# Optimization experiments

Measured on AMD Instinct MI355X. Metric: run time of the kernel, lower is better.

## Reference

```python
import jax, jax.numpy as jnp
import numpy as np

B, S, D, H, F, E, TOPK, W = 1, 4096, 768, 12, 3072, 7, 2, 256  # W = one-sided window


def _layer_norm(x, g, b, eps=1e-5):
    m = jnp.mean(x, -1, keepdims=True)
    v = jnp.var(x, -1, keepdims=True)
    return (x - m) * jax.lax.rsqrt(v + eps) * g + b


def _sliding_attn(x, Wq, bq, Wk, bk, Wv, bv):
    # Longformer sliding-window attention, chunked (no dense SxS matrix).
    Bx, Sx, Dx = x.shape
    Dh = Dx // H
    def proj(Wm, bm):
        return (x @ Wm + bm).reshape(Bx, Sx, H, Dh).transpose(0, 2, 1, 3)  # [B,H,S,Dh]
    q = proj(Wq, bq) * (1.0 / np.sqrt(Dh))
    k = proj(Wk, bk)
    v = proj(Wv, bv)
    nc = Sx // W
    kp = jnp.pad(k, ((0, 0), (0, 0), (W, W), (0, 0)))
    vp = jnp.pad(v, ((0, 0), (0, 0), (W, W), (0, 0)))
    # each query chunk of W tokens sees a 3W key window
    idx = (jnp.arange(nc) * W)[:, None] + jnp.arange(3 * W)[None, :]  # [nc,3W]
    kc = kp[:, :, idx]  # [B,H,nc,3W,Dh]
    vc = vp[:, :, idx]
    qc = q.reshape(Bx, H, nc, W, Dh)
    scores = jnp.einsum('bhcqd,bhckd->bhcqk', qc, kc)  # [B,H,nc,W,3W]
    qi = jnp.arange(W)[:, None]
    ki = jnp.arange(3 * W)[None, :]
    band = (ki >= qi) & (ki <= qi + 2 * W)  # |key_pos - query_pos| <= W
    pos = (jnp.arange(nc) * W)[:, None, None] + ki[None] - W  # global key pos
    valid = band[None] & (pos >= 0) & (pos < Sx)  # [nc,W,3W]
    scores = jnp.where(valid[None, None], scores, -1e9)
    probs = jax.nn.softmax(scores, axis=-1)
    out = jnp.einsum('bhcqk,bhckd->bhcqd', probs, vc)
    return out.reshape(Bx, H, Sx, Dh).transpose(0, 2, 1, 3).reshape(Bx, Sx, Dx)


def setup_inputs() -> dict:
    key = jax.random.key(0)
    ks = jax.random.split(key, 16)
    sc = 0.02
    rn = lambda k, shp: jax.random.normal(k, shp, jnp.float32) * sc
    return {
        'hidden_states': jax.random.normal(ks[0], (B, S, D), jnp.float32),
        'Wq': rn(ks[1], (D, D)), 'bq': jnp.zeros((D,), jnp.float32),
        'Wk': rn(ks[2], (D, D)), 'bk': jnp.zeros((D,), jnp.float32),
        'Wv': rn(ks[3], (D, D)), 'bv': jnp.zeros((D,), jnp.float32),
        'Wo': rn(ks[4], (D, D)), 'bo': jnp.zeros((D,), jnp.float32),
        'ln1_g': jnp.ones((D,), jnp.float32), 'ln1_b': jnp.zeros((D,), jnp.float32),
        'gate_W': rn(ks[5], (D, E)), 'gate_b': jnp.zeros((E,), jnp.float32),
        'W1e': rn(ks[6], (E, D, F)), 'b1e': jnp.zeros((E, F), jnp.float32),
        'W2e': rn(ks[7], (E, F, D)), 'b2e': jnp.zeros((E, D), jnp.float32),
        'Wd': rn(ks[8], (D, D)), 'bd': jnp.zeros((D,), jnp.float32),
        'ln2_g': jnp.ones((D,), jnp.float32), 'ln2_b': jnp.zeros((D,), jnp.float32),
    }


def reference(hidden_states, Wq, bq, Wk, bk, Wv, bv, Wo, bo, ln1_g, ln1_b,
              gate_W, gate_b, W1e, b1e, W2e, b2e, Wd, bd, ln2_g, ln2_b):
    # attention + SelfOutput (dense + residual + LN); dropout = identity (eval)
    attn = _sliding_attn(hidden_states, Wq, bq, Wk, bk, Wv, bv)
    attention_output = _layer_norm(attn @ Wo + bo + hidden_states, ln1_g, ln1_b)
    # MoE feed-forward: dense all-experts compute, top-k masked softmax gate
    gate_logits = attention_output @ gate_W + gate_b  # [B,S,E]
    topv, topi = jax.lax.top_k(gate_logits, TOPK)
    # softmax over (-inf scatter of topk) == softmax over topk values scattered back
    sw = jax.nn.softmax(topv, axis=-1)  # [B,S,k]
    gate_weights = jnp.einsum('bske,bsk->bse',
                              jax.nn.one_hot(topi, E, dtype=attention_output.dtype), sw)
    h = jax.nn.gelu(jnp.einsum('bsd,edf->bsef', attention_output, W1e) + b1e,
                    approximate=False)  # [B,S,E,F]
    eo = jnp.einsum('bsef,efd->bsed', h, W2e) + b2e  # [B,S,E,D]
    moe = jnp.einsum('bsed,bse->bsd', eo, gate_weights)
    ffn = moe @ Wd + bd
    layer_output = _layer_norm(ffn + attention_output, ln2_g, ln2_b)
    return layer_output, gate_weights
```

## Files before the change

### kernel.cpp

```cpp
#include <hip/hip_runtime.h>
#include <math.h>

#define S_LEN 4096
#define DMODEL 768
#define NHEADS 12
#define DH 64
#define FDIM 3072
#define NEXP 7
#define NPAIR (2*S_LEN)
#define MAXTILES 40

typedef _Float16 f16x8 __attribute__((ext_vector_type(8)));
typedef float f32x4 __attribute__((ext_vector_type(4)));

__device__ __forceinline__ unsigned short f2h(float f){
  union { _Float16 h; unsigned short u; } v; v.h = (_Float16)f; return v.u;
}
__device__ __forceinline__ float gelu_f(float x){
  return 0.5f * x * (1.0f + erff(x * 0.7071067811865475f));
}
__device__ __forceinline__ f32x4 mfma16(f16x8 a, f16x8 b, f32x4 c){
  return __builtin_amdgcn_mfma_f32_16x16x32_f16(a, b, c, 0, 0, 0);
}
__device__ __forceinline__ void glds16(const void* g, void* l){
  __builtin_amdgcn_global_load_lds((const __attribute__((address_space(1))) unsigned*)g,
                                   (__attribute__((address_space(3))) unsigned*)l, 16, 0, 0);
}

__global__ __launch_bounds__(256) void split_kernel(const float* __restrict__ in,
    unsigned short* __restrict__ out, int n){
  int i = blockIdx.x*256 + threadIdx.x;
  if (i >= n) return;
  out[i] = f2h(in[i]);
}

__global__ __launch_bounds__(256) void transp_kernel(const float* __restrict__ in,
    unsigned short* __restrict__ out,
    int R, int C, long inStride, long outStride){
  const float* ip = in + (long)blockIdx.z * inStride;
  long ob = (long)blockIdx.z * outStride;
  __shared__ float tile[32][33];
  int c0 = blockIdx.x*32, r0 = blockIdx.y*32;
  int tx = threadIdx.x, ty = threadIdx.y;
  for (int i = ty; i < 32; i += 8)
    tile[i][tx] = ip[(long)(r0+i)*C + c0 + tx];
  __syncthreads();
  int t  = tx + ty*32;
  int sx = t & 15;
  int sc = t >> 4;
  #pragma unroll
  for (int j = 0; j < 2; j++){
    int cc = sc + j*16;
    float v0 = tile[sx*2][cc], v1 = tile[sx*2+1][cc];
    long oidx = ob + (long)(c0+cc)*R + r0 + sx*2;
    unsigned uh = (unsigned)f2h(v0) | ((unsigned)f2h(v1) << 16);
    *(unsigned*)(out + oidx) = uh;
  }
}

struct GemmP {
  const unsigned short* A;
  const unsigned short* B;
  int M, N, K;
  const float* bias;  const float* bias2; const float* bias3;
  const float* resid;
  float* outF;
  unsigned short* outBF;
  unsigned short *qh,*kh,*vth;
  const int* pair_token;
  const float* pair_w;
  const int* cnt;
  const int* offs;
  const int* tile_e;
  const int* tile_m;
  const int* ntiles;
};

template<int MODE>
__global__ __launch_bounds__(256, 2) void gemm_bt(GemmP p){
  const int tid  = threadIdx.x;
  const int lane = tid & 63;
  const int wave = tid >> 6;
  const int quad = lane >> 4;
  const int ln   = lane & 15;
  const int wr = wave >> 1, wc = wave & 1;
  const int bn0 = blockIdx.x * 128;
  const int bm0 = blockIdx.y * 128;
  const int K = p.K;

  long aoff[2]; long boff[2]; int koff[2];
  #pragma unroll
  for (int j = 0; j < 2; j++){
    int c = tid + j*256;
    int row = c >> 2;
    koff[j] = (c & 3) * 8;
    aoff[j] = (long)(bm0 + row) * K;
    boff[j] = (long)(bn0 + row) * K;
  }

  __shared__ __align__(16) unsigned short As[2][128*32];
  __shared__ __align__(16) unsigned short Bs[2][128*32];

  auto stage = [&](int k0, int buf){
    #pragma unroll
    for (int j = 0; j < 2; j++){
      int c = tid + j*256;
      glds16(p.A + aoff[j] + k0 + koff[j], &As[buf][c*8]);
      glds16(p.B + boff[j] + k0 + koff[j], &Bs[buf][c*8]);
    }
  };

  f32x4 zero4 = {0.f, 0.f, 0.f, 0.f};
  f32x4 acc[4][4];
  #pragma unroll
  for (int i = 0; i < 4; i++)
    #pragma unroll
    for (int j = 0; j < 4; j++) acc[i][j] = zero4;

  stage(0, 0);
  __syncthreads();
  int cur = 0;

  for (int k0 = 0; k0 < K; k0 += 32){
    if (k0 + 32 < K) stage(k0 + 32, cur ^ 1);
    f16x8 af[4], bfr[4];
    #pragma unroll
    for (int mt = 0; mt < 4; mt++)
      af[mt] = *(const f16x8*)&As[cur][(wr*64 + mt*16 + ln)*32 + quad*8];
    #pragma unroll
    for (int nt = 0; nt < 4; nt++)
      bfr[nt] = *(const f16x8*)&Bs[cur][(wc*64 + nt*16 + ln)*32 + quad*8];
    #pragma unroll
    for (int mt = 0; mt < 4; mt++)
      #pragma unroll
      for (int nt = 0; nt < 4; nt++)
        acc[mt][nt] = mfma16(af[mt], bfr[nt], acc[mt][nt]);
    __syncthreads();
    cur ^= 1;
  }

  #pragma unroll
  for (int mt = 0; mt < 4; mt++){
    #pragma unroll
    for (int nt = 0; nt < 4; nt++){
      #pragma unroll
      for (int r = 0; r < 4; r++){
        int gm = bm0 + wr*64 + mt*16 + quad*4 + r;
        int gn = bn0 + wc*64 + nt*16 + ln;
        float v = acc[mt][nt][r];
        if (MODE == 0){
          int which = gn >= 1536 ? 2 : (gn >= 768 ? 1 : 0);
          int nn = gn - which*768;
          int hh = nn >> 6, dh = nn & 63;
          if (which == 0){
            float q = (v + p.bias[nn]) * 0.125f;
            long o = ((long)hh*S_LEN + gm)*64 + dh;
            p.qh[o] = f2h(q);
          } else if (which == 1){
            float kv = v + p.bias2[nn];
            long o = ((long)hh*S_LEN + gm)*64 + dh;
            p.kh[o] = f2h(kv);
          } else {
            float vv = v + p.bias3[nn];
            long o = ((long)hh*64 + dh)*S_LEN + gm;
            p.vth[o] = f2h(vv);
          }
        } else if (MODE == 1 || MODE == 4){
          long i = (long)gm*DMODEL + gn;
          p.outF[i] = v + p.bias[gn] + p.resid[i];
        }
      }
    }
  }
}

template<int MODE>
__global__ __launch_bounds__(512, 4) void gemm_big(GemmP p){
  const int ty = blockIdx.y;
  if (ty >= *p.ntiles) return;
  const int e   = p.tile_e[ty];
  const int bm0 = p.tile_m[ty];

  const int tid  = threadIdx.x;
  const int lane = tid & 63;
  const int wave = tid >> 6;
  const int quad = lane >> 4;
  const int ln   = lane & 15;
  const int wr = wave >> 1, wc = wave & 1;
  const int bn0 = blockIdx.x * 128;
  const int K = p.K;

  const int eoff = p.offs[e];
  const int Mloc = p.cnt[e];
  const unsigned short* Bp = p.B + (long)e * FDIM * DMODEL;

  long aoff[2]; int koffA[2];
  #pragma unroll
  for (int j = 0; j < 2; j++){
    int c = tid + j*512;
    int row = c >> 2;
    koffA[j] = (c & 3) * 8;
    int r = bm0 + row; if (r >= Mloc) r = Mloc - 1;
    aoff[j] = (MODE == 2) ? (long)p.pair_token[eoff + r] * K : (long)(eoff + r) * K;
  }
  long boff; int koffB;
  {
    int row = tid >> 2;
    koffB = (tid & 3) * 8;
    boff = (long)(bn0 + row) * K;
  }

  __shared__ __align__(16) unsigned short As[2][256*32];
  __shared__ __align__(16) unsigned short Bs[2][128*32];

  auto stage = [&](int k0, int buf){
    #pragma unroll
    for (int j = 0; j < 2; j++){
      int c = tid + j*512;
      glds16(p.A + aoff[j] + k0 + koffA[j], &As[buf][c*8]);
    }
    glds16(Bp + boff + k0 + koffB, &Bs[buf][tid*8]);
  };

  f32x4 zero4 = {0.f, 0.f, 0.f, 0.f};
  f32x4 acc[4][4];
  #pragma unroll
  for (int i = 0; i < 4; i++)
    #pragma unroll
    for (int j = 0; j < 4; j++) acc[i][j] = zero4;

  stage(0, 0);
  __syncthreads();
  int cur = 0;

  for (int k0 = 0; k0 < K; k0 += 32){
    if (k0 + 32 < K) stage(k0 + 32, cur ^ 1);
    f16x8 af[4], bfr[4];
    #pragma unroll
    for (int mt = 0; mt < 4; mt++)
      af[mt] = *(const f16x8*)&As[cur][(wr*64 + mt*16 + ln)*32 + quad*8];
    #pragma unroll
    for (int nt = 0; nt < 4; nt++)
      bfr[nt] = *(const f16x8*)&Bs[cur][(wc*64 + nt*16 + ln)*32 + quad*8];
    #pragma unroll
    for (int mt = 0; mt < 4; mt++)
      #pragma unroll
      for (int nt = 0; nt < 4; nt++)
        acc[mt][nt] = mfma16(af[mt], bfr[nt], acc[mt][nt]);
    __syncthreads();
    cur ^= 1;
  }

  #pragma unroll
  for (int mt = 0; mt < 4; mt++){
    #pragma unroll
    for (int nt = 0; nt < 4; nt++){
      #pragma unroll
      for (int r = 0; r < 4; r++){
        int gm = bm0 + wr*64 + mt*16 + quad*4 + r;
        int gn = bn0 + wc*64 + nt*16 + ln;
        if (gm < Mloc){
          float v = acc[mt][nt][r];
          if (MODE == 2){
            v = gelu_f(v + p.bias[(long)e*FDIM + gn]);
            p.outBF[(long)(eoff + gm)*FDIM + gn] = f2h(v);
          } else {
            int pi = eoff + gm;
            p.outF[(long)pi*DMODEL + gn] = v + p.bias[(long)e*DMODEL + gn];
          }
        }
      }
    }
  }
}

__global__ __launch_bounds__(256) void attn_mfma(
    const unsigned short* __restrict__ Qh,
    const unsigned short* __restrict__ Kh,
    const unsigned short* __restrict__ Vth,
    unsigned short* __restrict__ attn_h){
  const int c = blockIdx.x, h = blockIdx.y, qb = blockIdx.z;
  const int tid = threadIdx.x;
  const int lane = tid & 63, w = tid >> 6;
  const int quad = lane >> 4, ln = lane & 15;
  const int q0 = c*256 + qb*64;
  const int qw = q0 + w*16;

  __shared__ __align__(16) unsigned short Ks[64*64];
  __shared__ __align__(16) unsigned short Vs[64*64];
  __shared__ __align__(16) unsigned short Ps[4][16*72];

  f16x8 qf[2];
  {
    long qrow = ((long)h*S_LEN + qw + ln)*64 + quad*8;
    qf[0] = *(const f16x8*)(Qh + qrow);
    qf[1] = *(const f16x8*)(Qh + qrow + 32);
  }

  float m_s[4], l_s[4];
  f32x4 Oc[4];
  f32x4 z4 = {0.f,0.f,0.f,0.f};
  #pragma unroll
  for (int r = 0; r < 4; r++){ m_s[r] = -1e30f; l_s[r] = 0.f; }
  #pragma unroll
  for (int nt = 0; nt < 4; nt++) Oc[nt] = z4;

  const unsigned short* KB = Kh + (long)h*S_LEN*64;
  const unsigned short* VB = Vth + (long)h*64*S_LEN;

  for (int kb = 0; kb < 12; kb++){
    const int kstart = c*256 - 256 + kb*64;
    if (kstart + 63 < 0 || kstart >= S_LEN) continue;
    if (kstart + 63 < q0 - 256 || kstart > q0 + 63 + 256) continue;
    __syncthreads();
    #pragma unroll
    for (int p2 = 0; p2 < 2; p2++){
      int idx = p2*256 + tid;
      int row = idx >> 3;
      int pc  = idx & 7;
      int lc  = pc ^ (row & 7);
      int ka = kstart + row;
      int kac = ka < 0 ? 0 : (ka > S_LEN-1 ? S_LEN-1 : ka);
      long gK = (long)kac*64 + lc*8;
      glds16(KB + gK, &Ks[idx*8]);
      int ks0 = kstart + lc*8;
      ks0 = ks0 < 0 ? 0 : (ks0 > S_LEN-8 ? S_LEN-8 : ks0);
      long gV = (long)row*S_LEN + ks0;
      glds16(VB + gV, &Vs[idx*8]);
    }
    __syncthreads();
    if (kstart + 63 < qw - 256 || kstart > qw + 15 + 256) continue;

    f32x4 Sc[4];
    #pragma unroll
    for (int nt = 0; nt < 4; nt++) Sc[nt] = z4;
    #pragma unroll
    for (int kc = 0; kc < 2; kc++){
      f16x8 bh[4];
      #pragma unroll
      for (int nt = 0; nt < 4; nt++){
        int row = nt*16 + ln;
        int o = row*64 + (((kc*4 + quad) ^ (row & 7))*8);
        bh[nt] = *(const f16x8*)&Ks[o];
      }
      #pragma unroll
      for (int nt = 0; nt < 4; nt++)
        Sc[nt] = mfma16(qf[kc], bh[nt], Sc[nt]);
    }
    bool interior = (kstart >= qw - 241) && (kstart <= qw + 193) &&
                    (kstart >= 0) && (kstart + 63 <= S_LEN - 1);
    if (!interior){
      #pragma unroll
      for (int nt = 0; nt < 4; nt++){
        int ka = kstart + nt*16 + ln;
        #pragma unroll
        for (int r = 0; r < 4; r++){
          int qa = qw + quad*4 + r;
          bool v = (ka >= 0) && (ka < S_LEN) && (ka >= qa - 256) && (ka <= qa + 256);
          if (!v) Sc[nt][r] = -3.0e38f;
        }
      }
    }
    float bm[4];
    #pragma unroll
    for (int r = 0; r < 4; r++)
      bm[r] = fmaxf(fmaxf(Sc[0][r], Sc[1][r]), fmaxf(Sc[2][r], Sc[3][r]));
    #pragma unroll
    for (int off = 1; off < 16; off <<= 1)
      #pragma unroll
      for (int r = 0; r < 4; r++) bm[r] = fmaxf(bm[r], __shfl_xor(bm[r], off));
    float al[4];
    #pragma unroll
    for (int r = 0; r < 4; r++){
      float mnew = fmaxf(m_s[r], bm[r]);
      al[r] = __expf(m_s[r] - mnew);
      m_s[r] = mnew;
    }
    float psum[4] = {0.f,0.f,0.f,0.f};
    #pragma unroll
    for (int nt = 0; nt < 4; nt++){
      #pragma unroll
      for (int r = 0; r < 4; r++){
        float pv = __expf(Sc[nt][r] - m_s[r]);
        psum[r] += pv;
        int o = (quad*4 + r)*72 + nt*16 + ln;
        Ps[w][o] = f2h(pv);
      }
    }
    #pragma unroll
    for (int off = 1; off < 16; off <<= 1)
      #pragma unroll
      for (int r = 0; r < 4; r++) psum[r] += __shfl_xor(psum[r], off);
    #pragma unroll
    for (int r = 0; r < 4; r++) l_s[r] = l_s[r]*al[r] + psum[r];
    #pragma unroll
    for (int nt = 0; nt < 4; nt++)
      #pragma unroll
      for (int r = 0; r < 4; r++) Oc[nt][r] *= al[r];
    asm volatile("s_waitcnt lgkmcnt(0)" ::: "memory");
    #pragma unroll
    for (int kc = 0; kc < 2; kc++){
      f16x8 ph = *(const f16x8*)&Ps[w][ln*72 + kc*32 + quad*8];
      #pragma unroll
      for (int nt = 0; nt < 4; nt++){
        int row = nt*16 + ln;
        int o = row*64 + (((kc*4 + quad) ^ (row & 7))*8);
        f16x8 vh = *(const f16x8*)&Vs[o];
        Oc[nt] = mfma16(ph, vh, Oc[nt]);
      }
    }
  }
  float inv[4];
  #pragma unroll
  for (int r = 0; r < 4; r++) inv[r] = 1.f / l_s[r];
  #pragma unroll
  for (int nt = 0; nt < 4; nt++){
    #pragma unroll
    for (int r = 0; r < 4; r++){
      int qa = qw + quad*4 + r;
      long o = (long)qa*DMODEL + h*64 + nt*16 + ln;
      attn_h[o] = f2h(Oc[nt][r] * inv[r]);
    }
  }
}

__global__ __launch_bounds__(256) void ln_kernel(const float* __restrict__ x,
    const float* __restrict__ g, const float* __restrict__ b,
    float* __restrict__ outF, unsigned short* __restrict__ outH){
  int s = blockIdx.x;
  const float* row = x + (long)s*DMODEL;
  int t = threadIdx.x;
  float v0 = row[t], v1 = row[t+256], v2 = row[t+512];
  float sum = v0+v1+v2;
  float sq  = v0*v0 + v1*v1 + v2*v2;
  for (int o = 32; o > 0; o >>= 1){ sum += __shfl_xor(sum, o); sq += __shfl_xor(sq, o); }
  __shared__ float s1[4], s2[4];
  int wv = t >> 6;
  if ((t & 63) == 0){ s1[wv] = sum; s2[wv] = sq; }
  __syncthreads();
  sum = s1[0]+s1[1]+s1[2]+s1[3];
  sq  = s2[0]+s2[1]+s2[2]+s2[3];
  float mean = sum * (1.0f/DMODEL);
  float var  = sq  * (1.0f/DMODEL) - mean*mean;
  float inv = rsqrtf(var + 1e-5f);
  float* orow = outF + (long)s*DMODEL;
  unsigned short* hrow = outH ? outH + (long)s*DMODEL : (unsigned short*)0;
  #pragma unroll
  for (int j = 0; j < 3; j++){
    int d = t + j*256;
    float y = (row[d] - mean) * inv * g[d] + b[d];
    orow[d] = y;
    if (hrow) hrow[d] = f2h(y);
  }
}

__global__ __launch_bounds__(256) void gate_kernel(const float* __restrict__ x,
    const float* __restrict__ gw, const float* __restrict__ gb,
    float* __restrict__ gate_out, int* __restrict__ tok_e,
    float* __restrict__ tok_w){
  int w = threadIdx.x >> 6;
  int lane = threadIdx.x & 63;
  int s = blockIdx.x*4 + w;
  float acc[NEXP];
  #pragma unroll
  for (int e = 0; e < NEXP; e++) acc[e] = 0.f;
  const float* xr = x + (long)s*DMODEL;
  #pragma unroll
  for (int j = 0; j < DMODEL/64; j++){
    int d = lane + j*64;
    float xv = xr[d];
    const float* wr = gw + (long)d*NEXP;
    #pragma unroll
    for (int e = 0; e < NEXP; e++) acc[e] += xv * wr[e];
  }
  #pragma unroll
  for (int e = 0; e < NEXP; e++){
    float v = acc[e];
    for (int o = 32; o > 0; o >>= 1) v += __shfl_xor(v, o);
    acc[e] = v;
  }
  if (lane == 0){
    #pragma unroll
    for (int e = 0; e < NEXP; e++) acc[e] += gb[e];
    int i0 = 0;
    for (int e = 1; e < NEXP; e++) if (acc[e] > acc[i0]) i0 = e;
    int i1 = -1;
    for (int e = 0; e < NEXP; e++) if (e != i0 && (i1 < 0 || acc[e] > acc[i1])) i1 = e;
    float e1 = expf(acc[i1] - acc[i0]);
    float inv = 1.f / (1.f + e1);
    float w0 = inv, w1 = e1 * inv;
    float* go = gate_out + (long)s*NEXP;
    #pragma unroll
    for (int e = 0; e < NEXP; e++) go[e] = 0.f;
    go[i0] = w0; go[i1] = w1;
    tok_e[s*2] = i0; tok_e[s*2+1] = i1;
    tok_w[s*2] = w0; tok_w[s*2+1] = w1;
  }
}

__global__ __launch_bounds__(256) void route_kernel(const int* __restrict__ tok_e,
    const float* __restrict__ tok_w,
    int* __restrict__ cnt, int* __restrict__ offs,
    int* __restrict__ pair_token, float* __restrict__ pair_w, int* __restrict__ tok_pi,
    int* __restrict__ tile_e, int* __restrict__ tile_m, int* __restrict__ ntiles){
  __shared__ int hist[256][NEXP];
  __shared__ int cntS[NEXP], offsS[NEXP];
  const int t = threadIdx.x;
  const int CH = NPAIR/256;
  const int base = t*CH;
  #pragma unroll
  for (int e = 0; e < NEXP; e++) hist[t][e] = 0;
  for (int i = 0; i < CH; i++)
    hist[t][tok_e[base+i]]++;
  __syncthreads();
  if (t < NEXP){
    int s = 0;
    for (int i = 0; i < 256; i++){ int v = hist[i][t]; hist[i][t] = s; s += v; }
    cntS[t] = s;
  }
  __syncthreads();
  if (t == 0){
    int s = 0, tt = 0;
    for (int e = 0; e < NEXP; e++){ offsS[e] = s; s += cntS[e]; }
    for (int e = 0; e < NEXP; e++)
      for (int m0 = 0; m0 < cntS[e]; m0 += 256){ tile_e[tt] = e; tile_m[tt] = m0; tt++; }
    *ntiles = tt;
    for (int e = 0; e < NEXP; e++){ cnt[e] = cntS[e]; offs[e] = offsS[e]; }
  }
  __syncthreads();
  for (int i = 0; i < CH; i++){
    int idx = base + i;
    int e = tok_e[idx];
    int pi = offsS[e] + hist[t][e]++;
    pair_token[pi] = idx >> 1;
    pair_w[pi] = tok_w[idx];
    tok_pi[idx] = pi;
  }
}

__global__ __launch_bounds__(256) void combine_kernel(const float* __restrict__ Pbuf,
    const int* __restrict__ tok_pi, const float* __restrict__ tok_w,
    unsigned short* __restrict__ moe_h){
  int t = blockIdx.x;
  int d = threadIdx.x;
  float w0 = tok_w[t*2], w1 = tok_w[t*2+1];
  long p0 = (long)tok_pi[t*2]   * DMODEL;
  long p1 = (long)tok_pi[t*2+1] * DMODEL;
  unsigned short* orow = moe_h + (long)t*DMODEL;
  #pragma unroll
  for (int j = 0; j < 3; j++){
    int dd = d + j*256;
    orow[dd] = f2h(w0*Pbuf[p0+dd] + w1*Pbuf[p1+dd]);
  }
}

extern "C" void kernel_launch(void* const* d_in, const int* in_sizes, int n_in,
                              void* d_out, int out_size, void* d_ws, size_t ws_size,
                              hipStream_t stream){
  (void)in_sizes; (void)n_in; (void)out_size; (void)ws_size;
  const float* hidden = (const float*)d_in[0];
  const float* Wq  = (const float*)d_in[1];
  const float* bq  = (const float*)d_in[2];
  const float* Wk  = (const float*)d_in[3];
  const float* bk  = (const float*)d_in[4];
  const float* Wv  = (const float*)d_in[5];
  const float* bv  = (const float*)d_in[6];
  const float* Wo  = (const float*)d_in[7];
  const float* bo  = (const float*)d_in[8];
  const float* ln1g = (const float*)d_in[9];
  const float* ln1b = (const float*)d_in[10];
  const float* gateW = (const float*)d_in[11];
  const float* gateB = (const float*)d_in[12];
  const float* W1e = (const float*)d_in[13];
  const float* b1e = (const float*)d_in[14];
  const float* W2e = (const float*)d_in[15];
  const float* b2e = (const float*)d_in[16];
  const float* Wd  = (const float*)d_in[17];
  const float* bd  = (const float*)d_in[18];
  const float* ln2g = (const float*)d_in[19];
  const float* ln2b = (const float*)d_in[20];

  float* outL = (float*)d_out;
  float* outG = outL + (size_t)S_LEN*DMODEL;

  const size_t SD = (size_t)S_LEN*DMODEL;
  char* base = (char*)d_ws;
  size_t off = 0;
  auto alloc = [&](size_t bytes)->void*{
    void* r = base + off;
    off = (off + bytes + 255) & ~(size_t)255;
    return r;
  };
  unsigned short* x_h     = (unsigned short*)alloc(SD*2);
  unsigned short* wqkv_h  = (unsigned short*)alloc((size_t)2304*768*2);
  unsigned short* wo_h    = (unsigned short*)alloc((size_t)768*768*2);
  unsigned short* wd_h    = (unsigned short*)alloc((size_t)768*768*2);
  unsigned short* w1_h    = (unsigned short*)alloc((size_t)NEXP*FDIM*DMODEL*2);
  unsigned short* w2_h    = (unsigned short*)alloc((size_t)NEXP*FDIM*DMODEL*2);
  unsigned short* q_h   = (unsigned short*)alloc(SD*2);
  unsigned short* k_h   = (unsigned short*)alloc(SD*2);
  unsigned short* vt_h  = (unsigned short*)alloc(SD*2);
  unsigned short* attn_h = (unsigned short*)alloc(SD*2);
  float* preLN1    = (float*)alloc(SD*4);
  float* attnout_f = (float*)alloc(SD*4);
  unsigned short* attnout_h = (unsigned short*)alloc(SD*2);
  int*   tok_e = (int*)alloc(2*S_LEN*4);
  float* tok_w = (float*)alloc(2*S_LEN*4);
  int*   tok_pi = (int*)alloc(2*S_LEN*4);
  int*   cnt   = (int*)alloc(32*4);
  int*   offs  = (int*)alloc(32*4);
  int*   tile_e = (int*)alloc(MAXTILES*4);
  int*   tile_m = (int*)alloc(MAXTILES*4);
  int*   ntiles = (int*)alloc(4);
  int*   pair_token = (int*)alloc(NPAIR*4);
  float* pair_w     = (float*)alloc(NPAIR*4);
  unsigned short* Hbuf = (unsigned short*)alloc((size_t)NPAIR*FDIM*2);
  float* Pbuf = (float*)alloc((size_t)NPAIR*DMODEL*4);
  unsigned short* moe_h = (unsigned short*)alloc(SD*2);
  float* preLN2 = preLN1;

  split_kernel<<<dim3((unsigned)(SD/256)), dim3(256), 0, stream>>>(hidden, x_h, (int)SD);
  transp_kernel<<<dim3(24,24,1), dim3(32,8), 0, stream>>>(Wq, wqkv_h,           DMODEL, DMODEL, 0, 0);
  transp_kernel<<<dim3(24,24,1), dim3(32,8), 0, stream>>>(Wk, wqkv_h+768*768,   DMODEL, DMODEL, 0, 0);
  transp_kernel<<<dim3(24,24,1), dim3(32,8), 0, stream>>>(Wv, wqkv_h+2*768*768, DMODEL, DMODEL, 0, 0);
  transp_kernel<<<dim3(24,24,1), dim3(32,8), 0, stream>>>(Wo, wo_h, DMODEL, DMODEL, 0, 0);
  transp_kernel<<<dim3(24,24,1), dim3(32,8), 0, stream>>>(Wd, wd_h, DMODEL, DMODEL, 0, 0);
  transp_kernel<<<dim3(96,24,NEXP), dim3(32,8), 0, stream>>>(W1e, w1_h, DMODEL, FDIM, (long)DMODEL*FDIM, (long)DMODEL*FDIM);
  transp_kernel<<<dim3(24,96,NEXP), dim3(32,8), 0, stream>>>(W2e, w2_h, FDIM, DMODEL, (long)DMODEL*FDIM, (long)DMODEL*FDIM);

  GemmP pq = {};
  pq.A = x_h; pq.B = wqkv_h;
  pq.M = S_LEN; pq.N = 2304; pq.K = DMODEL;
  pq.bias = bq; pq.bias2 = bk; pq.bias3 = bv;
  pq.qh = q_h; pq.kh = k_h; pq.vth = vt_h;
  gemm_bt<0><<<dim3(18,32,1), dim3(256), 0, stream>>>(pq);

  attn_mfma<<<dim3(16,NHEADS,4), dim3(256), 0, stream>>>(q_h, k_h, vt_h, attn_h);

  GemmP pw = {};
  pw.A = attn_h; pw.B = wo_h;
  pw.M = S_LEN; pw.N = DMODEL; pw.K = DMODEL;
  pw.bias = bo; pw.resid = hidden; pw.outF = preLN1;
  gemm_bt<1><<<dim3(6,32,1), dim3(256), 0, stream>>>(pw);

  ln_kernel<<<dim3(S_LEN), dim3(256), 0, stream>>>(preLN1, ln1g, ln1b, attnout_f, attnout_h);

  gate_kernel<<<dim3(S_LEN/4), dim3(256), 0, stream>>>(attnout_f, gateW, gateB, outG, tok_e, tok_w);
  route_kernel<<<dim3(1), dim3(256), 0, stream>>>(tok_e, tok_w, cnt, offs,
      pair_token, pair_w, tok_pi, tile_e, tile_m, ntiles);

  GemmP p1 = {};
  p1.A = attnout_h; p1.B = w1_h; p1.M = S_LEN; p1.N = FDIM; p1.K = DMODEL;
  p1.bias = b1e; p1.outBF = Hbuf;
  p1.pair_token = pair_token; p1.cnt = cnt; p1.offs = offs;
  p1.tile_e = tile_e; p1.tile_m = tile_m; p1.ntiles = ntiles;
  gemm_big<2><<<dim3(24,MAXTILES), dim3(512), 0, stream>>>(p1);

  GemmP p2 = {};
  p2.A = Hbuf; p2.B = w2_h; p2.M = S_LEN; p2.N = DMODEL; p2.K = FDIM;
  p2.bias = b2e; p2.outF = Pbuf;
  p2.pair_token = pair_token; p2.pair_w = pair_w; p2.cnt = cnt; p2.offs = offs;
  p2.tile_e = tile_e; p2.tile_m = tile_m; p2.ntiles = ntiles;
  gemm_big<3><<<dim3(6,MAXTILES), dim3(512), 0, stream>>>(p2);

  combine_kernel<<<dim3(S_LEN), dim3(256), 0, stream>>>(Pbuf, tok_pi, tok_w, moe_h);
  GemmP pd = {};
  pd.A = moe_h; pd.B = wd_h; pd.M = S_LEN; pd.N = DMODEL; pd.K = DMODEL;
  pd.bias = bd; pd.resid = attnout_f; pd.outF = preLN2;
  gemm_bt<4><<<dim3(6,32,1), dim3(256), 0, stream>>>(pd);

  ln_kernel<<<dim3(S_LEN), dim3(256), 0, stream>>>(preLN2, ln2g, ln2b, outL, nullptr);
}
```

Before: 609.5 us.

## Deepen GEMM prefetch pipeline, swizzle LDS layout, and remap blocks across XCDs

Both GEMM kernels now prefetch two K-steps ahead, using explicit vmcnt waits and split barriers in place of a single __syncthreads. That lets global-to-LDS loads overlap MFMA work instead of draining every iteration. The K-chunk offset within each LDS row is XOR-swizzled by row to reduce bank conflicts on the fragment reads. Block indices are also remapped so neighbouring tiles land on the same XCD for better L2 reuse. The hand-written waitcnt counts are fragile and assume the grid size divides by 8.

```diff
diff --git a/kernel.cpp b/kernel.cpp
--- a/kernel.cpp
+++ b/kernel.cpp
@@ -25,6 +25,10 @@
 __device__ __forceinline__ void glds16(const void* g, void* l){
   __builtin_amdgcn_global_load_lds((const __attribute__((address_space(1))) unsigned*)g,
                                    (__attribute__((address_space(3))) unsigned*)l, 16, 0, 0);
+}
+__device__ __forceinline__ int xcd_logical(int lin, int total){
+  int q = total >> 3;
+  return (lin & 7)*q + (lin >> 3);
 }
 
 __global__ __launch_bounds__(256) void split_kernel(const float* __restrict__ in,
@@ -84,8 +88,10 @@
   const int quad = lane >> 4;
   const int ln   = lane & 15;
   const int wr = wave >> 1, wc = wave & 1;
-  const int bn0 = blockIdx.x * 128;
-  const int bm0 = blockIdx.y * 128;
+  const int lin = blockIdx.y * gridDim.x + blockIdx.x;
+  const int logical = xcd_logical(lin, gridDim.x*gridDim.y);
+  const int bn0 = (logical % gridDim.x) * 128;
+  const int bm0 = (logical / gridDim.x) * 128;
   const int K = p.K;
 
   long aoff[2]; long boff[2]; int koff[2];
@@ -93,7 +99,8 @@
   for (int j = 0; j < 2; j++){
     int c = tid + j*256;
     int row = c >> 2;
-    koff[j] = (c & 3) * 8;
+    int pc  = c & 3;
+    koff[j] = ((pc ^ (row & 3)) * 8);
     aoff[j] = (long)(bm0 + row) * K;
     boff[j] = (long)(bn0 + row) * K;
   }
@@ -118,24 +125,33 @@
     for (int j = 0; j < 4; j++) acc[i][j] = zero4;
 
   stage(0, 0);
-  __syncthreads();
+  stage(32, 1);
   int cur = 0;
 
   for (int k0 = 0; k0 < K; k0 += 32){
-    if (k0 + 32 < K) stage(k0 + 32, cur ^ 1);
+    if (k0 + 32 < K) { asm volatile("s_waitcnt vmcnt(4)" ::: "memory"); }
+    else             { asm volatile("s_waitcnt vmcnt(0)" ::: "memory"); }
+    __builtin_amdgcn_sched_barrier(0);
+    __builtin_amdgcn_s_barrier();
+
     f16x8 af[4], bfr[4];
     #pragma unroll
     for (int mt = 0; mt < 4; mt++)
-      af[mt] = *(const f16x8*)&As[cur][(wr*64 + mt*16 + ln)*32 + quad*8];
+      af[mt] = *(const f16x8*)&As[cur][(wr*64 + mt*16 + ln)*32 + ((quad ^ (ln & 3))*8)];
     #pragma unroll
     for (int nt = 0; nt < 4; nt++)
-      bfr[nt] = *(const f16x8*)&Bs[cur][(wc*64 + nt*16 + ln)*32 + quad*8];
+      bfr[nt] = *(const f16x8*)&Bs[cur][(wc*64 + nt*16 + ln)*32 + ((quad ^ (ln & 3))*8)];
+    asm volatile("s_waitcnt lgkmcnt(0)" ::: "memory");
+    __builtin_amdgcn_sched_barrier(0);
+    __builtin_amdgcn_s_barrier();
+
+    if (k0 + 64 < K) stage(k0 + 64, cur);
+
     #pragma unroll
     for (int mt = 0; mt < 4; mt++)
       #pragma unroll
       for (int nt = 0; nt < 4; nt++)
         acc[mt][nt] = mfma16(af[mt], bfr[nt], acc[mt][nt]);
-    __syncthreads();
     cur ^= 1;
   }
 
@@ -176,7 +192,10 @@
 
 template<int MODE>
 __global__ __launch_bounds__(512, 4) void gemm_big(GemmP p){
-  const int ty = blockIdx.y;
+  const int lin = blockIdx.y * gridDim.x + blockIdx.x;
+  const int logical = xcd_logical(lin, gridDim.x*gridDim.y);
+  const int bx = logical % gridDim.x;
+  const int ty = logical / gridDim.x;
   if (ty >= *p.ntiles) return;
   const int e   = p.tile_e[ty];
   const int bm0 = p.tile_m[ty];
@@ -187,7 +206,7 @@
   const int quad = lane >> 4;
   const int ln   = lane & 15;
   const int wr = wave >> 1, wc = wave & 1;
-  const int bn0 = blockIdx.x * 128;
+  const int bn0 = bx * 128;
   const int K = p.K;
 
   const int eoff = p.offs[e];
@@ -199,14 +218,16 @@
   for (int j = 0; j < 2; j++){
     int c = tid + j*512;
     int row = c >> 2;
-    koffA[j] = (c & 3) * 8;
+    int pc  = c & 3;
+    koffA[j] = ((pc ^ (row & 3)) * 8);
     int r = bm0 + row; if (r >= Mloc) r = Mloc - 1;
     aoff[j] = (MODE == 2) ? (long)p.pair_token[eoff + r] * K : (long)(eoff + r) * K;
   }
   long boff; int koffB;
   {
     int row = tid >> 2;
-    koffB = (tid & 3) * 8;
+    int pc  = tid & 3;
+    koffB = ((pc ^ (row & 3)) * 8);
     boff = (long)(bn0 + row) * K;
   }
 
@@ -230,24 +251,33 @@
     for (int j = 0; j < 4; j++) acc[i][j] = zero4;
 
   stage(0, 0);
-  __syncthreads();
+  stage(32, 1);
   int cur = 0;
 
   for (int k0 = 0; k0 < K; k0 += 32){
-    if (k0 + 32 < K) stage(k0 + 32, cur ^ 1);
+    if (k0 + 32 < K) { asm volatile("s_waitcnt vmcnt(3)" ::: "memory"); }
+    else             { asm volatile("s_waitcnt vmcnt(0)" ::: "memory"); }
+    __builtin_amdgcn_sched_barrier(0);
+    __builtin_amdgcn_s_barrier();
+
     f16x8 af[4], bfr[4];
     #pragma unroll
     for (int mt = 0; mt < 4; mt++)
-      af[mt] = *(const f16x8*)&As[cur][(wr*64 + mt*16 + ln)*32 + quad*8];
+      af[mt] = *(const f16x8*)&As[cur][(wr*64 + mt*16 + ln)*32 + ((quad ^ (ln & 3))*8)];
     #pragma unroll
     for (int nt = 0; nt < 4; nt++)
-      bfr[nt] = *(const f16x8*)&Bs[cur][(wc*64 + nt*16 + ln)*32 + quad*8];
+      bfr[nt] = *(const f16x8*)&Bs[cur][(wc*64 + nt*16 + ln)*32 + ((quad ^ (ln & 3))*8)];
+    asm volatile("s_waitcnt lgkmcnt(0)" ::: "memory");
+    __builtin_amdgcn_sched_barrier(0);
+    __builtin_amdgcn_s_barrier();
+
+    if (k0 + 64 < K) stage(k0 + 64, cur);
+
     #pragma unroll
     for (int mt = 0; mt < 4; mt++)
       #pragma unroll
       for (int nt = 0; nt < 4; nt++)
         acc[mt][nt] = mfma16(af[mt], bfr[nt], acc[mt][nt]);
-    __syncthreads();
     cur ^= 1;
   }
 
```

New measurement: 589.2 us. 1.03x faster.

## Unify GEMMs into one triple-buffered 256x128 kernel with XCD-aware block remap

Applied to the files above, without the earlier changes.

Replaces the separate dense and grouped-expert GEMM kernels with one templated kernel. It uses 256x128 output tiles computed by 4 waves, each covering 128x64. LDS gets three stages with explicit vmcnt waits and raw barriers, and register fragments are double-buffered so LDS reads for the next k-step overlap the current MFMAs. Block indices are remapped so neighbouring tiles land on the same XCD for L2 reuse, and s_setprio raises priority around the MFMA bursts. The costs are much higher register pressure, more LDS per block, and fewer blocks for the small 768-wide GEMMs.

```diff
diff --git a/kernel.cpp b/kernel.cpp
--- a/kernel.cpp
+++ b/kernel.cpp
@@ -25,6 +25,10 @@
 __device__ __forceinline__ void glds16(const void* g, void* l){
   __builtin_amdgcn_global_load_lds((const __attribute__((address_space(1))) unsigned*)g,
                                    (__attribute__((address_space(3))) unsigned*)l, 16, 0, 0);
+}
+__device__ __forceinline__ int xcd_logical(int lin, int total){
+  int q = total >> 3;
+  return (lin & 7)*q + (lin >> 3);
 }
 
 __global__ __launch_bounds__(256) void split_kernel(const float* __restrict__ in,
@@ -77,75 +81,135 @@
 };
 
 template<int MODE>
-__global__ __launch_bounds__(256, 2) void gemm_bt(GemmP p){
+__global__ __launch_bounds__(256, 2) void gemm_new(GemmP p){
   const int tid  = threadIdx.x;
   const int lane = tid & 63;
   const int wave = tid >> 6;
   const int quad = lane >> 4;
   const int ln   = lane & 15;
   const int wr = wave >> 1, wc = wave & 1;
-  const int bn0 = blockIdx.x * 128;
-  const int bm0 = blockIdx.y * 128;
-  const int K = p.K;
-
-  long aoff[2]; long boff[2]; int koff[2];
+
+  int bx, byy;
+  {
+    const int lin = blockIdx.y * gridDim.x + blockIdx.x;
+    const int logical = xcd_logical(lin, gridDim.x*gridDim.y);
+    bx  = logical % gridDim.x;
+    byy = logical / gridDim.x;
+  }
+  int e = 0, bm0, Mloc = 1<<30, eoff = 0;
+  const unsigned short* Bbase = p.B;
+  if (MODE == 2 || MODE == 3){
+    if (byy >= *p.ntiles) return;
+    e    = p.tile_e[byy];
+    bm0  = p.tile_m[byy];
+    eoff = p.offs[e];
+    Mloc = p.cnt[e];
+    Bbase = p.B + (long)e * FDIM * DMODEL;
+  } else {
+    bm0 = byy * 256;
+  }
+  const int bn0 = bx * 128;
+  const int K  = p.K;
+  const int nk = K >> 5;
+
+  long aoff[4]; int kca[4];
+  #pragma unroll
+  for (int j = 0; j < 4; j++){
+    int c = tid + j*256;
+    int row = c >> 2;
+    kca[j] = (c & 3) * 8;
+    int r = bm0 + row;
+    if (MODE == 2){ if (r >= Mloc) r = Mloc - 1; aoff[j] = (long)p.pair_token[eoff + r] * K; }
+    else if (MODE == 3){ if (r >= Mloc) r = Mloc - 1; aoff[j] = (long)(eoff + r) * K; }
+    else aoff[j] = (long)r * K;
+  }
+  long boff[2]; int kcb[2];
   #pragma unroll
   for (int j = 0; j < 2; j++){
     int c = tid + j*256;
     int row = c >> 2;
-    koff[j] = (c & 3) * 8;
-    aoff[j] = (long)(bm0 + row) * K;
+    kcb[j] = (c & 3) * 8;
     boff[j] = (long)(bn0 + row) * K;
   }
 
-  __shared__ __align__(16) unsigned short As[2][128*32];
-  __shared__ __align__(16) unsigned short Bs[2][128*32];
+  __shared__ __align__(16) unsigned short As[3][256*32];
+  __shared__ __align__(16) unsigned short Bs[3][128*32];
 
   auto stage = [&](int k0, int buf){
     #pragma unroll
-    for (int j = 0; j < 2; j++){
-      int c = tid + j*256;
-      glds16(p.A + aoff[j] + k0 + koff[j], &As[buf][c*8]);
-      glds16(p.B + boff[j] + k0 + koff[j], &Bs[buf][c*8]);
-    }
+    for (int j = 0; j < 4; j++)
+      glds16(p.A + aoff[j] + k0 + kca[j], &As[buf][(tid + j*256)*8]);
+    #pragma unroll
+    for (int j = 0; j < 2; j++)
+      glds16(Bbase + boff[j] + k0 + kcb[j], &Bs[buf][(tid + j*256)*8]);
   };
 
   f32x4 zero4 = {0.f, 0.f, 0.f, 0.f};
-  f32x4 acc[4][4];
-  #pragma unroll
-  for (int i = 0; i < 4; i++)
+  f32x4 acc[8][4];
+  #pragma unroll
+  for (int i = 0; i < 8; i++)
     #pragma unroll
     for (int j = 0; j < 4; j++) acc[i][j] = zero4;
 
   stage(0, 0);
-  __syncthreads();
-  int cur = 0;
-
-  for (int k0 = 0; k0 < K; k0 += 32){
-    if (k0 + 32 < K) stage(k0 + 32, cur ^ 1);
-    f16x8 af[4], bfr[4];
-    #pragma unroll
-    for (int mt = 0; mt < 4; mt++)
-      af[mt] = *(const f16x8*)&As[cur][(wr*64 + mt*16 + ln)*32 + quad*8];
-    #pragma unroll
-    for (int nt = 0; nt < 4; nt++)
-      bfr[nt] = *(const f16x8*)&Bs[cur][(wc*64 + nt*16 + ln)*32 + quad*8];
-    #pragma unroll
-    for (int mt = 0; mt < 4; mt++)
-      #pragma unroll
-      for (int nt = 0; nt < 4; nt++)
-        acc[mt][nt] = mfma16(af[mt], bfr[nt], acc[mt][nt]);
-    __syncthreads();
-    cur ^= 1;
-  }
-
-  #pragma unroll
-  for (int mt = 0; mt < 4; mt++){
+  stage(32, 1);
+  stage(64, 2);
+  asm volatile("s_waitcnt vmcnt(12)" ::: "memory");
+  __builtin_amdgcn_sched_barrier(0);
+  __builtin_amdgcn_s_barrier();
+  __builtin_amdgcn_sched_barrier(0);
+
+  f16x8 aC[8], bC[4], aN[8], bN[4];
+  #pragma unroll
+  for (int mt = 0; mt < 8; mt++)
+    aC[mt] = *(const f16x8*)&As[0][(wr*128 + mt*16 + ln)*32 + quad*8];
+  #pragma unroll
+  for (int nt = 0; nt < 4; nt++)
+    bC[nt] = *(const f16x8*)&Bs[0][(wc*64 + nt*16 + ln)*32 + quad*8];
+
+#define SUBITER(i, FCA, FCB, FNA, FNB) do { \
+    int s_ = t + (i); \
+    if (s_ + 1 < nk){ \
+      if (s_ + 2 < nk) { asm volatile("s_waitcnt vmcnt(6)" ::: "memory"); } \
+      else             { asm volatile("s_waitcnt vmcnt(0)" ::: "memory"); } \
+      asm volatile("s_waitcnt lgkmcnt(0)" ::: "memory"); \
+      __builtin_amdgcn_sched_barrier(0); \
+      __builtin_amdgcn_s_barrier(); \
+      __builtin_amdgcn_sched_barrier(0); \
+      if (s_ + 3 < nk) stage((s_+3)*32, (i)%3); \
+      _Pragma("unroll") \
+      for (int mt = 0; mt < 8; mt++) \
+        FNA[mt] = *(const f16x8*)&As[((i)+1)%3][(wr*128 + mt*16 + ln)*32 + quad*8]; \
+      _Pragma("unroll") \
+      for (int nt = 0; nt < 4; nt++) \
+        FNB[nt] = *(const f16x8*)&Bs[((i)+1)%3][(wc*64 + nt*16 + ln)*32 + quad*8]; \
+    } \
+    __builtin_amdgcn_s_setprio(1); \
+    _Pragma("unroll") \
+    for (int mt = 0; mt < 8; mt++) \
+      _Pragma("unroll") \
+      for (int nt = 0; nt < 4; nt++) \
+        acc[mt][nt] = mfma16(FCA[mt], FCB[nt], acc[mt][nt]); \
+    __builtin_amdgcn_s_setprio(0); \
+  } while(0)
+
+  for (int t = 0; t < nk; t += 6){
+    SUBITER(0, aC, bC, aN, bN);
+    SUBITER(1, aN, bN, aC, bC);
+    SUBITER(2, aC, bC, aN, bN);
+    SUBITER(3, aN, bN, aC, bC);
+    SUBITER(4, aC, bC, aN, bN);
+    SUBITER(5, aN, bN, aC, bC);
+  }
+#undef SUBITER
+
+  #pragma unroll
+  for (int mt = 0; mt < 8; mt++){
     #pragma unroll
     for (int nt = 0; nt < 4; nt++){
       #pragma unroll
       for (int r = 0; r < 4; r++){
-        int gm = bm0 + wr*64 + mt*16 + quad*4 + r;
+        int gm = bm0 + wr*128 + mt*16 + quad*4 + r;
         int gn = bn0 + wc*64 + nt*16 + ln;
         float v = acc[mt][nt][r];
         if (MODE == 0){
@@ -168,103 +232,13 @@
         } else if (MODE == 1 || MODE == 4){
           long i = (long)gm*DMODEL + gn;
           p.outF[i] = v + p.bias[gn] + p.resid[i];
-        }
-      }
-    }
-  }
-}
-
-template<int MODE>
-__global__ __launch_bounds__(512, 4) void gemm_big(GemmP p){
-  const int ty = blockIdx.y;
-  if (ty >= *p.ntiles) return;
-  const int e   = p.tile_e[ty];
-  const int bm0 = p.tile_m[ty];
-
-  const int tid  = threadIdx.x;
-  const int lane = tid & 63;
-  const int wave = tid >> 6;
-  const int quad = lane >> 4;
-  const int ln   = lane & 15;
-  const int wr = wave >> 1, wc = wave & 1;
-  const int bn0 = blockIdx.x * 128;
-  const int K = p.K;
-
-  const int eoff = p.offs[e];
-  const int Mloc = p.cnt[e];
-  const unsigned short* Bp = p.B + (long)e * FDIM * DMODEL;
-
-  long aoff[2]; int koffA[2];
-  #pragma unroll
-  for (int j = 0; j < 2; j++){
-    int c = tid + j*512;
-    int row = c >> 2;
-    koffA[j] = (c & 3) * 8;
-    int r = bm0 + row; if (r >= Mloc) r = Mloc - 1;
-    aoff[j] = (MODE == 2) ? (long)p.pair_token[eoff + r] * K : (long)(eoff + r) * K;
-  }
-  long boff; int koffB;
-  {
-    int row = tid >> 2;
-    koffB = (tid & 3) * 8;
-    boff = (long)(bn0 + row) * K;
-  }
-
-  __shared__ __align__(16) unsigned short As[2][256*32];
-  __shared__ __align__(16) unsigned short Bs[2][128*32];
-
-  auto stage = [&](int k0, int buf){
-    #pragma unroll
-    for (int j = 0; j < 2; j++){
-      int c = tid + j*512;
-      glds16(p.A + aoff[j] + k0 + koffA[j], &As[buf][c*8]);
-    }
-    glds16(Bp + boff + k0 + koffB, &Bs[buf][tid*8]);
-  };
-
-  f32x4 zero4 = {0.f, 0.f, 0.f, 0.f};
-  f32x4 acc[4][4];
-  #pragma unroll
-  for (int i = 0; i < 4; i++)
-    #pragma unroll
-    for (int j = 0; j < 4; j++) acc[i][j] = zero4;
-
-  stage(0, 0);
-  __syncthreads();
-  int cur = 0;
-
-  for (int k0 = 0; k0 < K; k0 += 32){
-    if (k0 + 32 < K) stage(k0 + 32, cur ^ 1);
-    f16x8 af[4], bfr[4];
-    #pragma unroll
-    for (int mt = 0; mt < 4; mt++)
-      af[mt] = *(const f16x8*)&As[cur][(wr*64 + mt*16 + ln)*32 + quad*8];
-    #pragma unroll
-    for (int nt = 0; nt < 4; nt++)
-      bfr[nt] = *(const f16x8*)&Bs[cur][(wc*64 + nt*16 + ln)*32 + quad*8];
-    #pragma unroll
-    for (int mt = 0; mt < 4; mt++)
-      #pragma unroll
-      for (int nt = 0; nt < 4; nt++)
-        acc[mt][nt] = mfma16(af[mt], bfr[nt], acc[mt][nt]);
-    __syncthreads();
-    cur ^= 1;
-  }
-
-  #pragma unroll
-  for (int mt = 0; mt < 4; mt++){
-    #pragma unroll
-    for (int nt = 0; nt < 4; nt++){
-      #pragma unroll
-      for (int r = 0; r < 4; r++){
-        int gm = bm0 + wr*64 + mt*16 + quad*4 + r;
-        int gn = bn0 + wc*64 + nt*16 + ln;
-        if (gm < Mloc){
-          float v = acc[mt][nt][r];
-          if (MODE == 2){
-            v = gelu_f(v + p.bias[(long)e*FDIM + gn]);
-            p.outBF[(long)(eoff + gm)*FDIM + gn] = f2h(v);
-          } else {
+        } else if (MODE == 2){
+          if (gm < Mloc){
+            float g = gelu_f(v + p.bias[(long)e*FDIM + gn]);
+            p.outBF[(long)(eoff + gm)*FDIM + gn] = f2h(g);
+          }
+        } else {
+          if (gm < Mloc){
             int pi = eoff + gm;
             p.outF[(long)pi*DMODEL + gn] = v + p.bias[(long)e*DMODEL + gn];
           }
@@ -633,7 +607,7 @@
   pq.M = S_LEN; pq.N = 2304; pq.K = DMODEL;
   pq.bias = bq; pq.bias2 = bk; pq.bias3 = bv;
   pq.qh = q_h; pq.kh = k_h; pq.vth = vt_h;
-  gemm_bt<0><<<dim3(18,32,1), dim3(256), 0, stream>>>(pq);
+  gemm_new<0><<<dim3(18,16,1), dim3(256), 0, stream>>>(pq);
 
   attn_mfma<<<dim3(16,NHEADS,4), dim3(256), 0, stream>>>(q_h, k_h, vt_h, attn_h);
 
@@ -641,7 +615,7 @@
   pw.A = attn_h; pw.B = wo_h;
   pw.M = S_LEN; pw.N = DMODEL; pw.K = DMODEL;
   pw.bias = bo; pw.resid = hidden; pw.outF = preLN1;
-  gemm_bt<1><<<dim3(6,32,1), dim3(256), 0, stream>>>(pw);
+  gemm_new<1><<<dim3(6,16,1), dim3(256), 0, stream>>>(pw);
 
   ln_kernel<<<dim3(S_LEN), dim3(256), 0, stream>>>(preLN1, ln1g, ln1b, attnout_f, attnout_h);
 
@@ -654,20 +628,20 @@
   p1.bias = b1e; p1.outBF = Hbuf;
   p1.pair_token = pair_token; p1.cnt = cnt; p1.offs = offs;
   p1.tile_e = tile_e; p1.tile_m = tile_m; p1.ntiles = ntiles;
-  gemm_big<2><<<dim3(24,MAXTILES), dim3(512), 0, stream>>>(p1);
+  gemm_new<2><<<dim3(24,MAXTILES), dim3(256), 0, stream>>>(p1);
 
   GemmP p2 = {};
   p2.A = Hbuf; p2.B = w2_h; p2.M = S_LEN; p2.N = DMODEL; p2.K = FDIM;
   p2.bias = b2e; p2.outF = Pbuf;
   p2.pair_token = pair_token; p2.pair_w = pair_w; p2.cnt = cnt; p2.offs = offs;
   p2.tile_e = tile_e; p2.tile_m = tile_m; p2.ntiles = ntiles;
-  gemm_big<3><<<dim3(6,MAXTILES), dim3(512), 0, stream>>>(p2);
+  gemm_new<3><<<dim3(6,MAXTILES), dim3(256), 0, stream>>>(p2);
 
   combine_kernel<<<dim3(S_LEN), dim3(256), 0, stream>>>(Pbuf, tok_pi, tok_w, moe_h);
   GemmP pd = {};
   pd.A = moe_h; pd.B = wd_h; pd.M = S_LEN; pd.N = DMODEL; pd.K = DMODEL;
   pd.bias = bd; pd.resid = attnout_f; pd.outF = preLN2;
-  gemm_bt<4><<<dim3(6,32,1), dim3(256), 0, stream>>>(pd);
+  gemm_new<4><<<dim3(6,16,1), dim3(256), 0, stream>>>(pd);
 
   ln_kernel<<<dim3(S_LEN), dim3(256), 0, stream>>>(preLN2, ln2g, ln2b, outL, nullptr);
 }
```

Measured after the change: 1.256 ms. 2.06x slower.
